# Kernel tuning notes

Measured on AMD Instinct MI355X. Metric: run time of the kernel, lower is better.

Reference implementation:

```python
import jax, jax.numpy as jnp
import numpy as np

GROUPS = 2
NUM_VARS = 320
VAR_DIM = 128  # vq_dim // groups = 256 // 2
CURR_TEMP = 2.0  # max_temp at num_updates=0
EPS = 1e-7


def setup_inputs() -> dict:
    key = jax.random.key(0)
    k1, k2, k3 = jax.random.split(key, 3)
    x = jax.random.normal(k1, (16, 2048, 768), dtype=jnp.float32)
    W = jax.random.normal(k2, (768, GROUPS * NUM_VARS), dtype=jnp.float32)  # std=1 per nn.init.normal_
    b = jnp.zeros((GROUPS * NUM_VARS,), dtype=jnp.float32)
    codebook = jax.random.uniform(k3, (1, GROUPS * NUM_VARS, VAR_DIM), dtype=jnp.float32)
    return {"x": x, "W": W, "b": b, "codebook": codebook}


def reference(x, W, b, codebook):
    # time_first=True -> x is [B, T, C]
    bsz, tsz, fsz = x.shape
    bt = bsz * tsz
    logits = x.reshape(bt, fsz) @ W + b                      # [BT, G*V]
    lg = logits.reshape(bt, GROUPS, NUM_VARS)                # [BT, G, V]

    # eval path: hard one-hot from argmax (self.training == False)
    k = jnp.argmax(lg, axis=-1)                              # [BT, G]
    hard = jax.nn.one_hot(k, NUM_VARS, dtype=logits.dtype)   # [BT, G, V]

    # codebook perplexity diagnostic
    avg_probs = jax.nn.softmax(lg.astype(jnp.float32), axis=-1).mean(axis=0)  # [G, V]
    ppl = jnp.exp(-jnp.sum(avg_probs * jnp.log(avg_probs + EPS), axis=-1)).sum()
    total_vars = GROUPS * NUM_VARS
    quantize_prob_ppl = (total_vars - ppl) / total_vars

    # one-hot x codebook multiply-sum == per-group gather, expressed as matmul
    cb = codebook.reshape(GROUPS, NUM_VARS, VAR_DIM)         # combine_groups=False
    q = jnp.einsum('ngv,gvd->ngd', hard, cb)                 # [BT, G, D]
    q = q.reshape(bsz, tsz, GROUPS * VAR_DIM)                # [B, T, vq_dim]
    return q, quantize_prob_ppl, jnp.float32(CURR_TEMP)
```

## Files before the change

kernel.cpp:

```cpp
#include <hip/hip_runtime.h>
#include <math.h>

#define GROUPS 2
#define NVARS  320
#define VDIM   128
#define NCOLS  640
#define FSZ    768
#define BTOT   32768
#define QDIM   256
#define KT     24
#define GAPTH  0.05f
#define LISTCAP 131072

typedef __bf16 bf16x8 __attribute__((ext_vector_type(8)));
typedef float  f32x4  __attribute__((ext_vector_type(4)));

__device__ __forceinline__ void gl_lds16(const void* g, void* l) {
    __builtin_amdgcn_global_load_lds(
        (const __attribute__((address_space(1))) unsigned int*)g,
        (__attribute__((address_space(3))) unsigned int*)l, 16, 0, 0);
}

__global__ __launch_bounds__(128) void xpre(
    const float* __restrict__ x, __bf16* __restrict__ xh, __bf16* __restrict__ xl, int row0)
{
    const int b = blockIdx.x;
    const int mblk = b / KT, kblk = b % KT;
    const int m = threadIdx.x;
    const float* src = x + (size_t)(row0 + mblk*128 + m) * FSZ + kblk*32;
    const size_t tbase = ((size_t)mblk*KT + kblk) * 4096;
    #pragma unroll
    for (int kq = 0; kq < 4; ++kq) {
        float4 a = ((const float4*)src)[kq*2];
        float4 c = ((const float4*)src)[kq*2+1];
        float vv[8] = {a.x,a.y,a.z,a.w,c.x,c.y,c.z,c.w};
        bf16x8 h, l;
        #pragma unroll
        for (int j = 0; j < 8; ++j) {
            __bf16 hh = (__bf16)vv[j];
            h[j] = hh;
            l[j] = (__bf16)(vv[j] - (float)hh);
        }
        ((bf16x8*)(xh + tbase))[kq*128 + m] = h;
        ((bf16x8*)(xl + tbase))[kq*128 + m] = l;
    }
}

__global__ __launch_bounds__(128) void wpre(
    const float* __restrict__ W, __bf16* __restrict__ wh, __bf16* __restrict__ wl)
{
    const int b = blockIdx.x;
    const int nblk = b / KT, kblk = b % KT;
    const int n = threadIdx.x;
    const size_t tbase = ((size_t)nblk*KT + kblk) * 4096;
    #pragma unroll
    for (int kq = 0; kq < 4; ++kq) {
        bf16x8 h, l;
        #pragma unroll
        for (int j = 0; j < 8; ++j) {
            float v = W[(size_t)(kblk*32 + kq*8 + j) * NCOLS + nblk*128 + n];
            __bf16 hh = (__bf16)v;
            h[j] = hh;
            l[j] = (__bf16)(v - (float)hh);
        }
        ((bf16x8*)(wh + tbase))[kq*128 + n] = h;
        ((bf16x8*)(wl + tbase))[kq*128 + n] = l;
    }
}

__global__ __launch_bounds__(256) void gemm_mfma(
    const __bf16* __restrict__ xh, const __bf16* __restrict__ xl,
    const __bf16* __restrict__ wh, const __bf16* __restrict__ wl,
    const float* __restrict__ bias, float* __restrict__ logits, int nwg)
{
    __shared__ __bf16 lds[16384];

    const int b = blockIdx.x;
    const int q8 = nwg >> 3, r8 = nwg & 7;
    const int xcd = b & 7, pos = b >> 3;
    const int L = (xcd < r8 ? xcd*(q8+1) : r8*(q8+1) + (xcd - r8)*q8) + pos;
    const int mblk = L / 5, nblk = L % 5;

    const int tid = threadIdx.x;
    const int w = tid >> 6, lane = tid & 63;
    const int wr = w >> 1, wc = w & 1;
    const int qq = lane >> 4, rr = lane & 15;

    f32x4 acc[4][4];
    #pragma unroll
    for (int i = 0; i < 4; ++i)
        #pragma unroll
        for (int j = 0; j < 4; ++j) acc[i][j] = (f32x4)0.f;

    const int ab = qq*128 + wr*64 + rr;
    const int bb = qq*128 + wc*64 + rr;

    for (int kt = 0; kt < KT; ++kt) {
        __syncthreads();
        const __bf16* ah_s = xh + ((size_t)mblk*KT + kt)*4096;
        const __bf16* al_s = xl + ((size_t)mblk*KT + kt)*4096;
        const __bf16* bh_s = wh + ((size_t)nblk*KT + kt)*4096;
        const __bf16* bl_s = wl + ((size_t)nblk*KT + kt)*4096;
        #pragma unroll
        for (int i = 0; i < 2; ++i) {
            const int u  = w*128 + i*64;
            const int el = (u + lane)*8;
            const int ed = u*8;
            gl_lds16(ah_s + el, &lds[0     + ed]);
            gl_lds16(al_s + el, &lds[4096  + ed]);
            gl_lds16(bh_s + el, &lds[8192  + ed]);
            gl_lds16(bl_s + el, &lds[12288 + ed]);
        }
        __syncthreads();

        const bf16x8* LAH = (const bf16x8*)&lds[0];
        const bf16x8* LAL = (const bf16x8*)&lds[4096];
        const bf16x8* LBH = (const bf16x8*)&lds[8192];
        const bf16x8* LBL = (const bf16x8*)&lds[12288];
        bf16x8 ah[4], al[4], bh[4], bl[4];
        #pragma unroll
        for (int mf = 0; mf < 4; ++mf) { ah[mf] = LAH[ab + mf*16]; al[mf] = LAL[ab + mf*16]; }
        #pragma unroll
        for (int nf = 0; nf < 4; ++nf) { bh[nf] = LBH[bb + nf*16]; bl[nf] = LBL[bb + nf*16]; }

        #pragma unroll
        for (int mf = 0; mf < 4; ++mf)
            #pragma unroll
            for (int nf = 0; nf < 4; ++nf) {
                acc[mf][nf] = __builtin_amdgcn_mfma_f32_16x16x32_bf16(ah[mf], bh[nf], acc[mf][nf], 0, 0, 0);
                acc[mf][nf] = __builtin_amdgcn_mfma_f32_16x16x32_bf16(al[mf], bh[nf], acc[mf][nf], 0, 0, 0);
                acc[mf][nf] = __builtin_amdgcn_mfma_f32_16x16x32_bf16(ah[mf], bl[nf], acc[mf][nf], 0, 0, 0);
            }
    }

    const int row0b = mblk*128 + wr*64;
    const int col0  = nblk*128 + wc*64;
    #pragma unroll
    for (int nf = 0; nf < 4; ++nf) {
        const int col = col0 + nf*16 + rr;
        const float bv = bias[col];
        #pragma unroll
        for (int mf = 0; mf < 4; ++mf) {
            const int rowb = row0b + mf*16 + qq*4;
            #pragma unroll
            for (int j = 0; j < 4; ++j)
                logits[(size_t)(rowb + j)*NCOLS + col] = acc[mf][nf][j] + bv;
        }
    }
}

#define RPB 16
__global__ __launch_bounds__(256) void rows_kernel(
    const float* __restrict__ logits, const float* __restrict__ cb,
    float* __restrict__ qout, float* __restrict__ partials,
    int* __restrict__ counter, int* __restrict__ list, int row0)
{
    __shared__ float probacc[4][NCOLS];
    const int tid = threadIdx.x, wid = tid >> 6, lane = tid & 63;
    for (int c = tid; c < 4*NCOLS; c += 256) ((float*)probacc)[c] = 0.f;
    __syncthreads();

    #pragma unroll
    for (int i = 0; i < RPB/4; ++i) {
        const int rl = blockIdx.x*RPB + wid*(RPB/4) + i;
        const float* lr = logits + (size_t)rl*NCOLS;
        const size_t grow = (size_t)row0 + rl;
        #pragma unroll
        for (int g = 0; g < GROUPS; ++g) {
            float v[5];
            #pragma unroll
            for (int j = 0; j < 5; ++j) v[j] = lr[g*NVARS + lane + 64*j];
            float m = v[0], m2 = -3.4e38f; int idx = lane;
            #pragma unroll
            for (int j = 1; j < 5; ++j) {
                if (v[j] > m) { m2 = m; m = v[j]; idx = lane + 64*j; }
                else m2 = fmaxf(m2, v[j]);
            }
            #pragma unroll
            for (int off = 32; off > 0; off >>= 1) {
                float om  = __shfl_xor(m, off);
                int   oi  = __shfl_xor(idx, off);
                float om2 = __shfl_xor(m2, off);
                if (om > m || (om == m && oi < idx)) { m2 = fmaxf(m, om2); m = om; idx = oi; }
                else m2 = fmaxf(m2, om);
            }
            float e[5], s = 0.f;
            #pragma unroll
            for (int j = 0; j < 5; ++j) { e[j] = expf(v[j] - m); s += e[j]; }
            #pragma unroll
            for (int off = 32; off > 0; off >>= 1) s += __shfl_xor(s, off);
            const float inv = 1.0f / s;
            #pragma unroll
            for (int j = 0; j < 5; ++j)
                probacc[wid][g*NVARS + lane + 64*j] += e[j] * inv;
            if (lane == 0 && (m - m2) < GAPTH) {
                int p = atomicAdd(counter, 1);
                if (p < LISTCAP) list[p] = ((int)grow << 1) | g;
            }
            const float2* srcc = (const float2*)(cb + (size_t)(g*NVARS + idx)*VDIM);
            float2* dst = (float2*)(qout + grow*QDIM + (size_t)g*VDIM);
            dst[lane] = srcc[lane];
        }
    }
    __syncthreads();
    const size_t pb = (size_t)(row0 >> 4) + blockIdx.x;
    for (int c = tid; c < NCOLS; c += 256)
        partials[pb*NCOLS + c] = probacc[0][c] + probacc[1][c] + probacc[2][c] + probacc[3][c];
}

__global__ __launch_bounds__(256) void fixup_kernel(
    const float* __restrict__ x, const float* __restrict__ W,
    const float* __restrict__ bias, const float* __restrict__ cb,
    float* __restrict__ qout, const int* __restrict__ counter, const int* __restrict__ list)
{
    __shared__ float red[4][NVARS];
    int cnt = *counter; if (cnt > LISTCAP) cnt = LISTCAP;
    const int tid = threadIdx.x, w = tid >> 6, lane = tid & 63;

    for (int e = blockIdx.x; e < cnt; e += gridDim.x) {
        const int ent = list[e];
        const int row = ent >> 1, g = ent & 1;
        const float* xr = x + (size_t)row*FSZ;

        float acc[5] = {0.f, 0.f, 0.f, 0.f, 0.f};
        for (int k0 = w*192; k0 < w*192 + 192; k0 += 4) {
            const float4 xv = *(const float4*)(xr + k0);
            const float xs[4] = {xv.x, xv.y, xv.z, xv.w};
            #pragma unroll
            for (int kk = 0; kk < 4; ++kk) {
                const float* wrow = W + (size_t)(k0 + kk)*NCOLS + g*NVARS;
                #pragma unroll
                for (int j = 0; j < 5; ++j)
                    acc[j] = fmaf(xs[kk], wrow[lane + 64*j], acc[j]);
            }
        }
        __syncthreads();
        #pragma unroll
        for (int j = 0; j < 5; ++j) red[w][lane + 64*j] = acc[j];
        __syncthreads();

        float v[5];
        #pragma unroll
        for (int j = 0; j < 5; ++j) {
            const int c = lane + 64*j;
            v[j] = red[0][c] + red[1][c] + red[2][c] + red[3][c] + bias[g*NVARS + c];
        }
        float m = v[0]; int idx = lane;
        #pragma unroll
        for (int j = 1; j < 5; ++j) if (v[j] > m) { m = v[j]; idx = lane + 64*j; }
        #pragma unroll
        for (int off = 32; off > 0; off >>= 1) {
            float om = __shfl_xor(m, off);
            int   oi = __shfl_xor(idx, off);
            if (om > m || (om == m && oi < idx)) { m = om; idx = oi; }
        }
        if (w == 0) {
            const float2* srcc = (const float2*)(cb + (size_t)(g*NVARS + idx)*VDIM);
            float2* dst = (float2*)(qout + (size_t)row*QDIM + (size_t)g*VDIM);
            dst[lane] = srcc[lane];
        }
    }
}

__global__ __launch_bounds__(64) void reduce_kernel(
    const float* __restrict__ partials, float* __restrict__ avg)
{
    const int c = blockIdx.x, lane = threadIdx.x;
    float s = 0.f;
    for (int p = lane; p < BTOT/RPB; p += 64) s += partials[(size_t)p*NCOLS + c];
    #pragma unroll
    for (int off = 32; off > 0; off >>= 1) s += __shfl_xor(s, off);
    if (lane == 0) avg[c] = s;
}

__global__ __launch_bounds__(64) void finalize_kernel(
    const float* __restrict__ avg, float* __restrict__ out)
{
    const int lane = threadIdx.x;
    float pp[GROUPS];
    #pragma unroll
    for (int g = 0; g < GROUPS; ++g) {
        float s = 0.f;
        #pragma unroll
        for (int j = 0; j < 5; ++j) {
            float p = avg[g*NVARS + lane + 64*j] * (1.0f/(float)BTOT);
            s += p * logf(p + 1e-7f);
        }
        #pragma unroll
        for (int off = 32; off > 0; off >>= 1) s += __shfl_xor(s, off);
        pp[g] = expf(-s);
    }
    if (lane == 0) {
        float ppl = pp[0] + pp[1];
        out[(size_t)BTOT*QDIM]     = ((float)NCOLS - ppl) / (float)NCOLS;
        out[(size_t)BTOT*QDIM + 1] = 2.0f;
    }
}

extern "C" void kernel_launch(void* const* d_in, const int* in_sizes, int n_in,
                              void* d_out, int out_size, void* d_ws, size_t ws_size,
                              hipStream_t stream)
{
    const float* x  = (const float*)d_in[0];
    const float* W  = (const float*)d_in[1];
    const float* b  = (const float*)d_in[2];
    const float* cb = (const float*)d_in[3];
    float* out = (float*)d_out;

    char* ws = (char*)d_ws;
    int*   counter  = (int*)ws;
    float* avg      = (float*)(ws + 1024);
    int*   list     = (int*)(ws + 8192);
    float* partials = (float*)(ws + 532480);
    __bf16* wh      = (__bf16*)(ws + 5775360);
    __bf16* wl      = (__bf16*)(ws + 6758400);
    char* chunkbase = ws + 7741440;

    long long avail = (long long)ws_size - 7741440;
    long long rmax = avail / 5632;
    int R = (int)((rmax / 1024) * 1024);
    if (R < 1024) R = (int)((rmax / 128) * 128);
    if (R > BTOT) R = BTOT;
    if (R < 128) R = 128;

    hipMemsetAsync(counter, 0, 4, stream);
    wpre<<<5*KT, 128, 0, stream>>>(W, wh, wl);

    for (int row0 = 0; row0 < BTOT; row0 += R) {
        int Rc = BTOT - row0; if (Rc > R) Rc = R;
        const int nmb = Rc / 128;
        __bf16* xh = (__bf16*)chunkbase;
        __bf16* xl = xh + (size_t)nmb*KT*4096;
        float* logits = (float*)(xl + (size_t)nmb*KT*4096);

        xpre<<<nmb*KT, 128, 0, stream>>>(x, xh, xl, row0);
        const int nwg = nmb * 5;
        gemm_mfma<<<nwg, 256, 0, stream>>>(xh, xl, wh, wl, b, logits, nwg);
        rows_kernel<<<Rc/RPB, 256, 0, stream>>>(logits, cb, out, partials, counter, list, row0);
    }
    fixup_kernel<<<512, 256, 0, stream>>>(x, W, b, cb, out, counter, list);
    reduce_kernel<<<NCOLS, 64, 0, stream>>>(partials, avg);
    finalize_kernel<<<1, 64, 0, stream>>>(avg, out);
}
```

Before: 366.2 us.

## Coalesce partial reduction, balance chunk sizes, widen fixup unroll, use fast exp

The partials reduction changes from one block per column with strided reads to 16 blocks reading contiguous rows and atomically adding into avg, which is now zeroed by a larger memset. Chunk size R is now chosen to split the rows evenly across the minimum number of chunks instead of rounding down to a multiple of 1024, which reduces uneven tail chunks. The fixup loop is unrolled by 8 instead of 4, and the softmax uses __expf. Atomic float adds make the reduction order nondeterministic, and __expf slightly lowers precision.

```diff
diff --git a/kernel.cpp b/kernel.cpp
--- a/kernel.cpp
+++ b/kernel.cpp
@@ -186,7 +186,7 @@
             }
             float e[5], s = 0.f;
             #pragma unroll
-            for (int j = 0; j < 5; ++j) { e[j] = expf(v[j] - m); s += e[j]; }
+            for (int j = 0; j < 5; ++j) { e[j] = __expf(v[j] - m); s += e[j]; }
             #pragma unroll
             for (int off = 32; off > 0; off >>= 1) s += __shfl_xor(s, off);
             const float inv = 1.0f / s;
@@ -223,11 +223,12 @@
         const float* xr = x + (size_t)row*FSZ;
 
         float acc[5] = {0.f, 0.f, 0.f, 0.f, 0.f};
-        for (int k0 = w*192; k0 < w*192 + 192; k0 += 4) {
-            const float4 xv = *(const float4*)(xr + k0);
-            const float xs[4] = {xv.x, xv.y, xv.z, xv.w};
-            #pragma unroll
-            for (int kk = 0; kk < 4; ++kk) {
+        for (int k0 = w*192; k0 < w*192 + 192; k0 += 8) {
+            const float4 xv0 = *(const float4*)(xr + k0);
+            const float4 xv1 = *(const float4*)(xr + k0 + 4);
+            const float xs[8] = {xv0.x, xv0.y, xv0.z, xv0.w, xv1.x, xv1.y, xv1.z, xv1.w};
+            #pragma unroll
+            for (int kk = 0; kk < 8; ++kk) {
                 const float* wrow = W + (size_t)(k0 + kk)*NCOLS + g*NVARS;
                 #pragma unroll
                 for (int j = 0; j < 5; ++j)
@@ -262,15 +263,26 @@
     }
 }
 
-__global__ __launch_bounds__(64) void reduce_kernel(
+#define REDBLK 16
+__global__ __launch_bounds__(256) void reduce_kernel(
     const float* __restrict__ partials, float* __restrict__ avg)
 {
-    const int c = blockIdx.x, lane = threadIdx.x;
-    float s = 0.f;
-    for (int p = lane; p < BTOT/RPB; p += 64) s += partials[(size_t)p*NCOLS + c];
-    #pragma unroll
-    for (int off = 32; off > 0; off >>= 1) s += __shfl_xor(s, off);
-    if (lane == 0) avg[c] = s;
+    const int tid = threadIdx.x;
+    const int p0 = blockIdx.x * (BTOT/RPB/REDBLK);
+    float s[3] = {0.f, 0.f, 0.f};
+    for (int p = p0; p < p0 + BTOT/RPB/REDBLK; ++p) {
+        const float* row = partials + (size_t)p*NCOLS;
+        #pragma unroll
+        for (int i = 0; i < 3; ++i) {
+            const int c = tid + i*256;
+            if (c < NCOLS) s[i] += row[c];
+        }
+    }
+    #pragma unroll
+    for (int i = 0; i < 3; ++i) {
+        const int c = tid + i*256;
+        if (c < NCOLS) atomicAdd(&avg[c], s[i]);
+    }
 }
 
 __global__ __launch_bounds__(64) void finalize_kernel(
@@ -318,12 +330,12 @@
 
     long long avail = (long long)ws_size - 7741440;
     long long rmax = avail / 5632;
-    int R = (int)((rmax / 1024) * 1024);
-    if (R < 1024) R = (int)((rmax / 128) * 128);
-    if (R > BTOT) R = BTOT;
-    if (R < 128) R = 128;
-
-    hipMemsetAsync(counter, 0, 4, stream);
+    if (rmax > BTOT) rmax = BTOT;
+    if (rmax < 128)  rmax = 128;
+    int chunks = (int)((BTOT + rmax - 1) / rmax);
+    int R = ((BTOT / chunks + 127) / 128) * 128;
+
+    hipMemsetAsync(ws, 0, 4096, stream);
     wpre<<<5*KT, 128, 0, stream>>>(W, wh, wl);
 
     for (int row0 = 0; row0 < BTOT; row0 += R) {
@@ -339,6 +351,6 @@
         rows_kernel<<<Rc/RPB, 256, 0, stream>>>(logits, cb, out, partials, counter, list, row0);
     }
     fixup_kernel<<<512, 256, 0, stream>>>(x, W, b, cb, out, counter, list);
-    reduce_kernel<<<NCOLS, 64, 0, stream>>>(partials, avg);
+    reduce_kernel<<<REDBLK, 256, 0, stream>>>(partials, avg);
     finalize_kernel<<<1, 64, 0, stream>>>(avg, out);
 }
```

After: 430.0 us. 1.17x slower.
